# Kernel tuning notes

Measured on AMD Instinct MI355X. Metric: run time of the kernel, lower is better.

## Reference

```python
import jax, jax.numpy as jnp
import numpy as np

BITS = 4            # OPU.bits
VEC = 64            # OPU.input_vector_len / weight_vector_len
QMAX = 2 ** (BITS - 1) - 1   # 7


def ste_round(x):
    # straight-through round (onn_round)
    return x + jax.lax.stop_gradient(jnp.round(x) - x)


@jax.custom_vjp
def onn_dot_sum(x, w):
    # x: [N, R, VEC], w: [VEC, R, M]
    # per-chunk matmul -> clamp to int8 range -> binarize (>=0 -> 1) -> sum over chunks
    s = jnp.einsum('nrc,crm->nrm', x, w)
    s = jnp.clip(s, -128.0, 127.0)
    return jnp.where(s < 0, 0.0, 1.0).sum(axis=1)  # [N, M]


def _onn_dot_fwd(x, w):
    return onn_dot_sum(x, w), (x, w)


def _onn_dot_bwd(res, g):
    # onn_dot_fun.backward: straight-through past clamp+threshold;
    # each chunk receives the same grad g (sum over chunks).
    x, w = res
    gx = jnp.einsum('nm,crm->nrc', g, w)
    gw = jnp.einsum('nrc,nm->crm', x, g)
    return gx, gw


onn_dot_sum.defvjp(_onn_dot_fwd, _onn_dot_bwd)


def _onn_conv2d(inp, weight):
    B, C, H, W = inp.shape
    Cout, Cin, k, _ = weight.shape
    pad = (k - 1) // 2  # SAME, stride=1
    # im2col (matches torch F.unfold channel-major ordering: C, kh, kw)
    xp = jnp.pad(inp, ((0, 0), (0, 0), (pad, pad), (pad, pad)))
    patches = jnp.stack([xp[:, :, i:i + H, j:j + W]
                         for i in range(k) for j in range(k)], axis=2)  # [B,C,k*k,H,W]
    inp_unf = patches.reshape(B, C * k * k, H * W).transpose(0, 2, 1)    # [B,L,D]
    # weight quantization: STE round + clamp to 4-bit signed range
    scale = (2 ** BITS - 1) / (weight.max() - weight.min() + 1e-9)
    wq = jnp.clip(ste_round(weight * scale), -QMAX, QMAX)
    w_ = wq.reshape(Cout, -1).T                                          # [D, Cout]
    D = C * k * k
    repeats = -(-D // VEC)
    padD = VEC * repeats - D
    x = jnp.pad(inp_unf, ((0, 0), (0, 0), (0, padD))).reshape(B * H * W, repeats, VEC)
    wpad = jnp.pad(w_, ((0, padD), (0, 0)))                              # [VEC*R, Cout]
    wr = wpad.T.reshape(Cout, repeats, VEC).transpose(2, 1, 0)           # [VEC,R,Cout]
    temp = onn_dot_sum(x, wr)                                            # [B*L, Cout]
    return temp.reshape(B, H * W, Cout).transpose(0, 2, 1).reshape(B, Cout, H, W)


def setup_inputs() -> dict:
    key = jax.random.key(0)
    k1, k2 = jax.random.split(key)
    B, Cin, H, W = 16, 128, 32, 32
    Cout, k = 256, 3
    inp = jax.random.normal(k1, (B, Cin, H, W), dtype=jnp.float32)
    fan_in = Cin * k * k
    bound = 1.0 / np.sqrt(fan_in)  # kaiming_uniform with a=sqrt(5)
    weight = jax.random.uniform(k2, (Cout, Cin, k, k), dtype=jnp.float32,
                                minval=-bound, maxval=bound)
    return {"inp": inp, "weight": weight}


def reference(inp, weight):
    return _onn_conv2d(inp, weight)
```

## Files before the change

### kernel.cpp

```cpp
#include <hip/hip_runtime.h>


#define TAU 0.03f
#define HITCAP 2048

typedef short short8 __attribute__((ext_vector_type(8)));
typedef float f32x4 __attribute__((ext_vector_type(4)));
typedef unsigned int uv4 __attribute__((ext_vector_type(4)));

__device__ __forceinline__ unsigned short bf16rn(float v) {
    unsigned u = __float_as_uint(v);
    unsigned r = u + 0x7fffu + ((u >> 16) & 1u);
    return (unsigned short)(r >> 16);
}

__global__ __launch_bounds__(256) void k_prep(const float* __restrict__ w,
                                              const float* __restrict__ inp,
                                              float* __restrict__ pmin,
                                              float* __restrict__ pmax,
                                              unsigned* __restrict__ xpk) {
    if (blockIdx.x < 64) {
        int tid = blockIdx.x * 256 + threadIdx.x;
        float vmin = 1e30f, vmax = -1e30f;
        for (int i = tid; i < 294912; i += 64 * 256) {
            float v = w[i];
            vmin = fminf(vmin, v);
            vmax = fmaxf(vmax, v);
        }
        #pragma unroll
        for (int off = 32; off > 0; off >>= 1) {
            vmin = fminf(vmin, __shfl_down(vmin, off, 64));
            vmax = fmaxf(vmax, __shfl_down(vmax, off, 64));
        }
        __shared__ float smin[4], smax[4];
        int wave = threadIdx.x >> 6;
        if ((threadIdx.x & 63) == 0) { smin[wave] = vmin; smax[wave] = vmax; }
        __syncthreads();
        if (threadIdx.x == 0) {
            #pragma unroll
            for (int i = 1; i < 4; i++) {
                vmin = fminf(vmin, smin[i]);
                vmax = fmaxf(vmax, smax[i]);
            }
            pmin[blockIdx.x] = vmin;
            pmax[blockIdx.x] = vmax;
        }
    } else {
        int bc = blockIdx.x - 64;
        const float* src = inp + (size_t)bc * 1024;
        unsigned* dst = xpk + (size_t)bc * 1156;
        #pragma unroll
        for (int i = 0; i < 5; ++i) {
            int idx = threadIdx.x + i * 256;
            if (idx < 1156) {
                int yy = idx / 34, xx = idx - yy * 34;
                float v = 0.0f;
                int ys = yy - 1, xs_ = xx - 1;
                if ((unsigned)ys < 32u && (unsigned)xs_ < 32u) v = src[ys * 32 + xs_];
                unsigned short h = bf16rn(v);
                float hf = __uint_as_float((unsigned)h << 16);
                unsigned short l = bf16rn(v - hf);
                dst[idx] = (unsigned)h | ((unsigned)l << 16);
            }
        }
    }
}

__device__ __forceinline__ float block_scale(const float* pmin, const float* pmax,
                                             float* sca_lds) {
    int t = threadIdx.x;
    if (t < 64) {
        float vmin = pmin[t];
        float vmax = pmax[t];
        #pragma unroll
        for (int off = 32; off > 0; off >>= 1) {
            vmin = fminf(vmin, __shfl_down(vmin, off, 64));
            vmax = fmaxf(vmax, __shfl_down(vmax, off, 64));
        }
        if (t == 0) {
            float tt = __fadd_rn(__fsub_rn(vmax, vmin), 1e-9f);
            *sca_lds = __fdiv_rn(15.0f, tt);
        }
    }
    __syncthreads();
    return *sca_lds;
}

__global__ __launch_bounds__(256) void k_quantb(const float* __restrict__ w,
                                                const float* __restrict__ pmin,
                                                const float* __restrict__ pmax,
                                                uv4* __restrict__ wqb) {
    __shared__ float sca;
    float s = block_scale(pmin, pmax, &sca);
    int slot = blockIdx.x * 256 + threadIdx.x;
    int lane = slot & 63;
    int sub = slot >> 6;
    int khalf = sub & 1;
    int mt = (sub >> 1) & 3;
    int gr = sub >> 3;
    int g = gr / 18, r = gr - g * 18;
    int m = g * 64 + mt * 16 + (lane & 15);
    int dbase = r * 64 + khalf * 32 + (lane >> 4) * 8;
    const float* wp = w + (size_t)m * 1152 + dbase;
    unsigned o[4];
    #pragma unroll
    for (int p = 0; p < 4; ++p) {
        float q0 = rintf(__fmul_rn(wp[2 * p], s));
        float q1 = rintf(__fmul_rn(wp[2 * p + 1], s));
        q0 = fminf(fmaxf(q0, -7.0f), 7.0f);
        q1 = fminf(fmaxf(q1, -7.0f), 7.0f);
        o[p] = (unsigned)bf16rn(q0) | ((unsigned)bf16rn(q1) << 16);
    }
    uv4 v; v.x = o[0]; v.y = o[1]; v.z = o[2]; v.w = o[3];
    wqb[slot] = v;
}

__global__ __launch_bounds__(256) void k_main(const unsigned* __restrict__ xpk,
                                              const uv4* __restrict__ wqb,
                                              const float* __restrict__ inp,
                                              const float* __restrict__ weight,
                                              const float* __restrict__ pmin,
                                              const float* __restrict__ pmax,
                                              float* __restrict__ out) {
    __shared__ int ofs_s[1152];
    __shared__ unsigned hitbuf[HITCAP];
    __shared__ unsigned hitcnt;
    __shared__ float sca;

    const int t = threadIdx.x;
    if (t == 0) hitcnt = 0u;
    float sc = block_scale(pmin, pmax, &sca);
    for (int k = t; k < 1152; k += 256) {
        int cin = k / 9;
        int rem = k - cin * 9;
        int kh = rem / 3;
        int kw = rem - kh * 3;
        ofs_s[k] = cin * 1156 + kh * 34 + kw;
    }
    __syncthreads();

    const int lane = t & 63;
    const int wv = t >> 6;
    const int quad = lane >> 4;
    const int nl = lane & 15;
    const int n0 = blockIdx.x * 64;
    const int g = blockIdx.y;
    const int b = n0 >> 10;

    const int sy_w = ((n0 & 1023) >> 5) + (wv >> 1);
    const int col0 = (wv & 1) * 16;
    const unsigned* __restrict__ xw =
        xpk + (size_t)b * (128 * 1156) + sy_w * 34 + col0 + nl;
    const uv4* __restrict__ aw = wqb + (size_t)g * (18 * 512) + lane;

    int counts[4][4] = {};

    unsigned pb[16];
    #pragma unroll
    for (int q2 = 0; q2 < 16; ++q2) {
        int k = (q2 >> 3) * 32 + quad * 8 + (q2 & 7);
        pb[q2] = xw[ofs_s[k]];
    }

    for (int r = 0; r < 18; ++r) {
        unsigned cb[16];
        #pragma unroll
        for (int q2 = 0; q2 < 16; ++q2) cb[q2] = pb[q2];
        if (r < 17) {
            #pragma unroll
            for (int q2 = 0; q2 < 16; ++q2) {
                int k = (r + 1) * 64 + (q2 >> 3) * 32 + quad * 8 + (q2 & 7);
                pb[q2] = xw[ofs_s[k]];
            }
        }

        short8 bhi[2], blo[2];
        #pragma unroll
        for (int kh2 = 0; kh2 < 2; ++kh2) {
            union { unsigned d[4]; short8 v; } H, L;
            #pragma unroll
            for (int p = 0; p < 4; ++p) {
                unsigned ua = cb[kh2 * 8 + 2 * p], ub = cb[kh2 * 8 + 2 * p + 1];
                H.d[p] = (ua & 0xffffu) | (ub << 16);
                L.d[p] = (ua >> 16) | (ub & 0xffff0000u);
            }
            bhi[kh2] = H.v;
            blo[kh2] = L.v;
        }

        #pragma unroll
        for (int mt = 0; mt < 4; ++mt) {
            short8 af0 = __builtin_bit_cast(short8, aw[r * 512 + (mt * 2 + 0) * 64]);
            short8 af1 = __builtin_bit_cast(short8, aw[r * 512 + (mt * 2 + 1) * 64]);
            f32x4 acc = {0.0f, 0.0f, 0.0f, 0.0f};
            acc = __builtin_amdgcn_mfma_f32_16x16x32_bf16(af0, bhi[0], acc, 0, 0, 0);
            acc = __builtin_amdgcn_mfma_f32_16x16x32_bf16(af1, bhi[1], acc, 0, 0, 0);
            acc = __builtin_amdgcn_mfma_f32_16x16x32_bf16(af0, blo[0], acc, 0, 0, 0);
            acc = __builtin_amdgcn_mfma_f32_16x16x32_bf16(af1, blo[1], acc, 0, 0, 0);
            #pragma unroll
            for (int i = 0; i < 4; ++i) {
                float s = acc[i];
                int ge = (s >= 0.0f) ? 1 : 0;
                counts[mt][i] += ge;
                if (__builtin_fabsf(s) < TAU) {
                    unsigned idx = atomicAdd(&hitcnt, 1u);
                    if (idx < (unsigned)HITCAP) {
                        unsigned m = (unsigned)(g * 64 + mt * 16 + quad * 4 + i);
                        unsigned n = (unsigned)(n0 + wv * 16 + nl);
                        hitbuf[idx] = n | ((unsigned)r << 14) | (m << 19) | ((unsigned)ge << 27);
                    }
                }
            }
        }
    }

    {
        const int n = n0 + wv * 16 + nl;
        const int p = n & 1023;
        #pragma unroll
        for (int mt = 0; mt < 4; ++mt)
            #pragma unroll
            for (int i = 0; i < 4; ++i) {
                int m = g * 64 + mt * 16 + quad * 4 + i;
                out[(((size_t)(b * 256 + m)) << 10) + p] = (float)counts[mt][i];
            }
    }

    __syncthreads();
    unsigned tot = hitcnt;
    if (tot > (unsigned)HITCAP) tot = (unsigned)HITCAP;
    for (unsigned i = t; i < tot; i += 256) {
        unsigned u = hitbuf[i];
        int n = u & 16383;
        int r = (u >> 14) & 31;
        int m = (u >> 19) & 255;
        int bit = (u >> 27) & 1;
        int bb = n >> 10, p = n & 1023, y = p >> 5, x = p & 31;
        const float* ib = inp + (size_t)bb * (128 * 32 * 32);
        const float* wp = weight + (size_t)m * 1152;
        float s = 0.0f;
        int d = r * 64;
        for (int c = 0; c < 64; ++c, ++d) {
            int ci = d / 9, rem = d - ci * 9;
            int kh = rem / 3, kw = rem - kh * 3;
            int yy = y + kh - 1, xx = x + kw - 1;
            float xv = 0.0f;
            if ((unsigned)yy < 32u && (unsigned)xx < 32u)
                xv = ib[(ci * 32 + yy) * 32 + xx];
            float q = rintf(__fmul_rn(wp[d], sc));
            q = fminf(fmaxf(q, -7.0f), 7.0f);
            s = __fadd_rn(s, __fmul_rn(xv, q));
        }
        int nb = (s >= 0.0f) ? 1 : 0;
        if (nb != bit)
            atomicAdd(&out[(((size_t)(bb * 256 + m)) << 10) + p], nb ? 1.0f : -1.0f);
    }
}

extern "C" void kernel_launch(void* const* d_in, const int* in_sizes, int n_in,
                              void* d_out, int out_size, void* d_ws, size_t ws_size,
                              hipStream_t stream) {
    const float* inp    = (const float*)d_in[0];
    const float* weight = (const float*)d_in[1];
    float* out = (float*)d_out;

    char* ws = (char*)d_ws;
    float*    pmin  = (float*)(ws + 0);
    float*    pmax  = (float*)(ws + 256);
    uv4*      wqb   = (uv4*)(ws + 1024);
    unsigned* xpk   = (unsigned*)(ws + 590848);

    k_prep<<<2112, 256, 0, stream>>>(weight, inp, pmin, pmax, xpk);
    k_quantb<<<144, 256, 0, stream>>>(weight, pmin, pmax, wqb);

    dim3 grid(256, 4);
    k_main<<<grid, 256, 0, stream>>>(xpk, wqb, inp, weight, pmin, pmax, out);
}
```

Measured before the change: 130.8 us.

## Fuse weight min/max reduction and quantization into the prep kernel

Merges the quantization kernel into the prep launch. Each quantization block recomputes the full weight min/max itself instead of relying on a separate partial-reduction pass. One block writes the final scale to workspace so the main kernel reads a single float instead of reducing partials. This removes one kernel launch and its dependency, but adds redundant reads of the whole weight tensor per quantization block.

```diff
diff --git a/kernel.cpp b/kernel.cpp
--- a/kernel.cpp
+++ b/kernel.cpp
@@ -16,42 +16,17 @@
 
 __global__ __launch_bounds__(256) void k_prep(const float* __restrict__ w,
                                               const float* __restrict__ inp,
-                                              float* __restrict__ pmin,
-                                              float* __restrict__ pmax,
-                                              unsigned* __restrict__ xpk) {
-    if (blockIdx.x < 64) {
-        int tid = blockIdx.x * 256 + threadIdx.x;
-        float vmin = 1e30f, vmax = -1e30f;
-        for (int i = tid; i < 294912; i += 64 * 256) {
-            float v = w[i];
-            vmin = fminf(vmin, v);
-            vmax = fmaxf(vmax, v);
-        }
-        #pragma unroll
-        for (int off = 32; off > 0; off >>= 1) {
-            vmin = fminf(vmin, __shfl_down(vmin, off, 64));
-            vmax = fmaxf(vmax, __shfl_down(vmax, off, 64));
-        }
-        __shared__ float smin[4], smax[4];
-        int wave = threadIdx.x >> 6;
-        if ((threadIdx.x & 63) == 0) { smin[wave] = vmin; smax[wave] = vmax; }
-        __syncthreads();
-        if (threadIdx.x == 0) {
-            #pragma unroll
-            for (int i = 1; i < 4; i++) {
-                vmin = fminf(vmin, smin[i]);
-                vmax = fmaxf(vmax, smax[i]);
-            }
-            pmin[blockIdx.x] = vmin;
-            pmax[blockIdx.x] = vmax;
-        }
-    } else {
-        int bc = blockIdx.x - 64;
+                                              float* __restrict__ scale_ws,
+                                              unsigned* __restrict__ xpk,
+                                              uv4* __restrict__ wqb) {
+    const int t = threadIdx.x;
+    if (blockIdx.x < 2048) {
+        int bc = blockIdx.x;
         const float* src = inp + (size_t)bc * 1024;
         unsigned* dst = xpk + (size_t)bc * 1156;
         #pragma unroll
         for (int i = 0; i < 5; ++i) {
-            int idx = threadIdx.x + i * 256;
+            int idx = t + i * 256;
             if (idx < 1156) {
                 int yy = idx / 34, xx = idx - yy * 34;
                 float v = 0.0f;
@@ -63,73 +38,72 @@
                 dst[idx] = (unsigned)h | ((unsigned)l << 16);
             }
         }
-    }
-}
-
-__device__ __forceinline__ float block_scale(const float* pmin, const float* pmax,
-                                             float* sca_lds) {
-    int t = threadIdx.x;
-    if (t < 64) {
-        float vmin = pmin[t];
-        float vmax = pmax[t];
+    } else {
+        float vmin = 1e30f, vmax = -1e30f;
+        for (int i = t; i < 294912; i += 256) {
+            float v = w[i];
+            vmin = fminf(vmin, v);
+            vmax = fmaxf(vmax, v);
+        }
         #pragma unroll
         for (int off = 32; off > 0; off >>= 1) {
             vmin = fminf(vmin, __shfl_down(vmin, off, 64));
             vmax = fmaxf(vmax, __shfl_down(vmax, off, 64));
         }
+        __shared__ float smin[4], smax[4], sca;
+        int wave = t >> 6;
+        if ((t & 63) == 0) { smin[wave] = vmin; smax[wave] = vmax; }
+        __syncthreads();
         if (t == 0) {
+            #pragma unroll
+            for (int i = 1; i < 4; i++) {
+                vmin = fminf(vmin, smin[i]);
+                vmax = fmaxf(vmax, smax[i]);
+            }
             float tt = __fadd_rn(__fsub_rn(vmax, vmin), 1e-9f);
-            *sca_lds = __fdiv_rn(15.0f, tt);
-        }
-    }
-    __syncthreads();
-    return *sca_lds;
-}
-
-__global__ __launch_bounds__(256) void k_quantb(const float* __restrict__ w,
-                                                const float* __restrict__ pmin,
-                                                const float* __restrict__ pmax,
-                                                uv4* __restrict__ wqb) {
-    __shared__ float sca;
-    float s = block_scale(pmin, pmax, &sca);
-    int slot = blockIdx.x * 256 + threadIdx.x;
-    int lane = slot & 63;
-    int sub = slot >> 6;
-    int khalf = sub & 1;
-    int mt = (sub >> 1) & 3;
-    int gr = sub >> 3;
-    int g = gr / 18, r = gr - g * 18;
-    int m = g * 64 + mt * 16 + (lane & 15);
-    int dbase = r * 64 + khalf * 32 + (lane >> 4) * 8;
-    const float* wp = w + (size_t)m * 1152 + dbase;
-    unsigned o[4];
-    #pragma unroll
-    for (int p = 0; p < 4; ++p) {
-        float q0 = rintf(__fmul_rn(wp[2 * p], s));
-        float q1 = rintf(__fmul_rn(wp[2 * p + 1], s));
-        q0 = fminf(fmaxf(q0, -7.0f), 7.0f);
-        q1 = fminf(fmaxf(q1, -7.0f), 7.0f);
-        o[p] = (unsigned)bf16rn(q0) | ((unsigned)bf16rn(q1) << 16);
-    }
-    uv4 v; v.x = o[0]; v.y = o[1]; v.z = o[2]; v.w = o[3];
-    wqb[slot] = v;
+            sca = __fdiv_rn(15.0f, tt);
+            if (blockIdx.x == 2048) *scale_ws = sca;
+        }
+        __syncthreads();
+        float s = sca;
+
+        int slot = (blockIdx.x - 2048) * 256 + t;
+        int lane = slot & 63;
+        int sub = slot >> 6;
+        int khalf = sub & 1;
+        int mt = (sub >> 1) & 3;
+        int gr = sub >> 3;
+        int g = gr / 18, r = gr - g * 18;
+        int m = g * 64 + mt * 16 + (lane & 15);
+        int dbase = r * 64 + khalf * 32 + (lane >> 4) * 8;
+        const float* wp = w + (size_t)m * 1152 + dbase;
+        unsigned o[4];
+        #pragma unroll
+        for (int p = 0; p < 4; ++p) {
+            float q0 = rintf(__fmul_rn(wp[2 * p], s));
+            float q1 = rintf(__fmul_rn(wp[2 * p + 1], s));
+            q0 = fminf(fmaxf(q0, -7.0f), 7.0f);
+            q1 = fminf(fmaxf(q1, -7.0f), 7.0f);
+            o[p] = (unsigned)bf16rn(q0) | ((unsigned)bf16rn(q1) << 16);
+        }
+        uv4 v; v.x = o[0]; v.y = o[1]; v.z = o[2]; v.w = o[3];
+        wqb[slot] = v;
+    }
 }
 
 __global__ __launch_bounds__(256) void k_main(const unsigned* __restrict__ xpk,
                                               const uv4* __restrict__ wqb,
                                               const float* __restrict__ inp,
                                               const float* __restrict__ weight,
-                                              const float* __restrict__ pmin,
-                                              const float* __restrict__ pmax,
+                                              const float* __restrict__ scale_ws,
                                               float* __restrict__ out) {
     __shared__ int ofs_s[1152];
     __shared__ unsigned hitbuf[HITCAP];
     __shared__ unsigned hitcnt;
-    __shared__ float sca;
 
     const int t = threadIdx.x;
     if (t == 0) hitcnt = 0u;
-    float sc = block_scale(pmin, pmax, &sca);
+    const float sc = *scale_ws;
     for (int k = t; k < 1152; k += 256) {
         int cin = k / 9;
         int rem = k - cin * 9;
@@ -265,14 +239,12 @@
     float* out = (float*)d_out;
 
     char* ws = (char*)d_ws;
-    float*    pmin  = (float*)(ws + 0);
-    float*    pmax  = (float*)(ws + 256);
+    float*    scale = (float*)(ws + 0);
     uv4*      wqb   = (uv4*)(ws + 1024);
     unsigned* xpk   = (unsigned*)(ws + 590848);
 
-    k_prep<<<2112, 256, 0, stream>>>(weight, inp, pmin, pmax, xpk);
-    k_quantb<<<144, 256, 0, stream>>>(weight, pmin, pmax, wqb);
+    k_prep<<<2192, 256, 0, stream>>>(weight, inp, scale, xpk, wqb);
 
     dim3 grid(256, 4);
-    k_main<<<grid, 256, 0, stream>>>(xpk, wqb, inp, weight, pmin, pmax, out);
-}
+    k_main<<<grid, 256, 0, stream>>>(xpk, wqb, inp, weight, scale, out);
+}
```

New measurement: 399.5 us. 3.06x slower.
